# Kernel tuning notes

Hardware: AMD Instinct MI355X
Metric: run time of the kernel (lower is better)

The kernel has to match this reference:

```python
import jax, jax.numpy as jnp
import numpy as np

N_NODES = 100000


def gcn_conv(x, edge_index, W, b):
    # PyG GCNConv: h = D^{-1/2} (A + I) D^{-1/2} (x @ W) + b
    N = x.shape[0]
    h = x @ W  # [N, C_out]
    loops = jnp.arange(N, dtype=edge_index.dtype)
    src = jnp.concatenate([edge_index[0], loops])
    dst = jnp.concatenate([edge_index[1], loops])
    deg = jax.ops.segment_sum(jnp.ones_like(dst, dtype=h.dtype), dst, num_segments=N)
    inv_sqrt = jnp.where(deg > 0, jax.lax.rsqrt(deg), 0.0)
    norm = inv_sqrt[src] * inv_sqrt[dst]              # [E+N]
    msg = h[src] * norm[:, None]                      # gather + scale
    out = jax.ops.segment_sum(msg, dst, num_segments=N)  # scatter-add
    return out + b


def setup_inputs() -> dict:
    key = jax.random.key(0)
    ks = jax.random.split(key, 6)
    x = jax.random.normal(ks[0], (N_NODES, 4), dtype=jnp.float32)
    edge_index = jax.random.randint(ks[1], (2, 3200000), 0, N_NODES, dtype=jnp.int32)
    edge_label_index = jax.random.randint(ks[2], (2, 200000), 0, N_NODES, dtype=jnp.int32)
    W1 = jax.random.normal(ks[3], (4, 128), dtype=jnp.float32) * (1.0 / np.sqrt(4))
    b1 = jnp.zeros((128,), dtype=jnp.float32)
    W2 = jax.random.normal(ks[4], (128, 64), dtype=jnp.float32) * (1.0 / np.sqrt(128))
    b2 = jnp.zeros((64,), dtype=jnp.float32)
    return {"x": x, "edge_index": edge_index, "edge_label_index": edge_label_index,
            "W1": W1, "b1": b1, "W2": W2, "b2": b2}


def reference(x, edge_index, edge_label_index, W1, b1, W2, b2):
    h = jax.nn.relu(gcn_conv(x, edge_index, W1, b1))
    z = gcn_conv(h, edge_index, W2, b2)               # encode -> [N, 64]
    # decode: dot product per labeled edge -> [E_lbl]
    logits = jnp.sum(z[edge_label_index[0]] * z[edge_label_index[1]], axis=-1)
    return logits
```

## Files before the change

### kernel.cpp

```cpp
#include <hip/hip_runtime.h>

#define N_NODES 100000
#define N_EDGES 3200000
#define N_LBL   200000
#define C1 128
#define C2 64

#define BSH   7
#define NPB   128
#define NBKT  ((N_NODES + NPB - 1) / NPB)
#define NCB   500
#define PPT   512
#define CHUNK (N_EDGES / NCB)
#define CAP   4992

#define RS    136

typedef _Float16 half8 __attribute__((ext_vector_type(8)));
typedef float    f32x4 __attribute__((ext_vector_type(4)));

__device__ __forceinline__ float4 f4add(float4 a, float4 b) {
    return make_float4(a.x + b.x, a.y + b.y, a.z + b.z, a.w + b.w);
}
__device__ __forceinline__ unsigned short f2bf(float f) {
    unsigned int u = __float_as_uint(f);
    u += 0x7fff + ((u >> 16) & 1);
    return (unsigned short)(u >> 16);
}
__device__ __forceinline__ float bflo(unsigned int u) {
    return __uint_as_float(u << 16);
}
__device__ __forceinline__ float bfhi(unsigned int u) {
    return __uint_as_float(u & 0xffff0000u);
}
__device__ __forceinline__ void acc16(float* acc, uint4 v) {
    acc[0] += bflo(v.x); acc[1] += bfhi(v.x);
    acc[2] += bflo(v.y); acc[3] += bfhi(v.y);
    acc[4] += bflo(v.z); acc[5] += bfhi(v.z);
    acc[6] += bflo(v.w); acc[7] += bfhi(v.w);
}

__global__ __launch_bounds__(PPT) void pair_place_kernel(const int* __restrict__ ei,
        int* __restrict__ gcursor, unsigned int* __restrict__ pairs) {
    __shared__ int hist[NBKT];
    __shared__ int cur[NBKT];
    __shared__ int lofs[NBKT];
    __shared__ unsigned int sortbuf[CHUNK];
    __shared__ unsigned short bkt16[CHUNK];
    int tid = threadIdx.x;
    for (int i = tid; i < NBKT; i += PPT) hist[i] = 0;
    __syncthreads();
    int base = blockIdx.x * CHUNK;
    unsigned int pk[13]; int bkt[13]; int rnk[13];
    int e0 = base + tid * 12;
    #pragma unroll
    for (int kk = 0; kk < 3; ++kk) {
        int4 sv = *(const int4*)(ei + e0 + kk * 4);
        int4 dv = *(const int4*)(ei + N_EDGES + e0 + kk * 4);
        int b0 = dv.x >> BSH, b1 = dv.y >> BSH;
        int b2 = dv.z >> BSH, b3 = dv.w >> BSH;
        bkt[kk * 4 + 0] = b0;
        pk[kk * 4 + 0] = ((unsigned int)(dv.x & (NPB - 1)) << 17) | (unsigned int)sv.x;
        rnk[kk * 4 + 0] = atomicAdd(&hist[b0], 1);
        bkt[kk * 4 + 1] = b1;
        pk[kk * 4 + 1] = ((unsigned int)(dv.y & (NPB - 1)) << 17) | (unsigned int)sv.y;
        rnk[kk * 4 + 1] = atomicAdd(&hist[b1], 1);
        bkt[kk * 4 + 2] = b2;
        pk[kk * 4 + 2] = ((unsigned int)(dv.z & (NPB - 1)) << 17) | (unsigned int)sv.z;
        rnk[kk * 4 + 2] = atomicAdd(&hist[b2], 1);
        bkt[kk * 4 + 3] = b3;
        pk[kk * 4 + 3] = ((unsigned int)(dv.w & (NPB - 1)) << 17) | (unsigned int)sv.w;
        rnk[kk * 4 + 3] = atomicAdd(&hist[b3], 1);
    }
    if (tid < 256) {
        int e = base + 6144 + tid;
        int s = ei[e], d = ei[N_EDGES + e];
        int b = d >> BSH;
        bkt[12] = b;
        pk[12] = ((unsigned int)(d & (NPB - 1)) << 17) | (unsigned int)s;
        rnk[12] = atomicAdd(&hist[b], 1);
    }
    __syncthreads();
    for (int i = tid; i < NBKT; i += PPT) {
        int h = hist[i];
        cur[i] = h ? (i * CAP + atomicAdd(&gcursor[i], h)) : 0;
    }
    if (tid < 64) {
        int beg = tid * 13;
        int en = min(beg + 13, NBKT);
        int s = 0;
        for (int i = beg; i < en; ++i) s += hist[i];
        int incl = s;
        #pragma unroll
        for (int off = 1; off < 64; off <<= 1) {
            int t = __shfl_up(incl, off);
            if (tid >= off) incl += t;
        }
        int excl = incl - s;
        for (int i = beg; i < en; ++i) {
            lofs[i] = excl;
            excl += hist[i];
        }
    }
    __syncthreads();
    #pragma unroll
    for (int k = 0; k < 12; ++k) {
        int p = lofs[bkt[k]] + rnk[k];
        sortbuf[p] = pk[k];
        bkt16[p] = (unsigned short)bkt[k];
    }
    if (tid < 256) {
        int p = lofs[bkt[12]] + rnk[12];
        sortbuf[p] = pk[12];
        bkt16[p] = (unsigned short)bkt[12];
    }
    __syncthreads();
    for (int j = tid; j < CHUNK; j += PPT) {
        int b = bkt16[j];
        int pos = cur[b] + (j - lofs[b]);
        pos = min(pos, NBKT * CAP - 1);
        pairs[pos] = sortbuf[j];
    }
}

__global__ __launch_bounds__(512) void bucket_finish_kernel(
        const unsigned int* __restrict__ pairs, const int* __restrict__ gcursor,
        const float4* __restrict__ x, int* __restrict__ offs, int* __restrict__ ends,
        float* __restrict__ inv, float4* __restrict__ xs, int* __restrict__ srcs) {
    __shared__ int deg[NPB];
    __shared__ int nstart[NPB];
    __shared__ int wsum2[2];
    __shared__ __align__(16) int ls[CAP];
    int tid = threadIdx.x;
    int b = blockIdx.x;
    int nbase = b << BSH;
    int eb = b * CAP;
    int cnt = min(gcursor[b], CAP);
    if (tid < NPB) deg[tid] = 0;
    __syncthreads();
    unsigned int pk[12]; int rnk[12];
    const uint4* pv = (const uint4*)(pairs + eb);
    #pragma unroll
    for (int kk = 0; kk < 3; ++kk) {
        int j4 = kk * 512 + tid;
        if (kk < 2 || j4 < CAP / 4) {
            uint4 p4 = pv[j4];
            int jb = j4 * 4;
            if (jb < cnt) {
                pk[kk * 4 + 0] = p4.x;
                rnk[kk * 4 + 0] = atomicAdd(&deg[p4.x >> 17], 1);
            }
            if (jb + 1 < cnt) {
                pk[kk * 4 + 1] = p4.y;
                rnk[kk * 4 + 1] = atomicAdd(&deg[p4.y >> 17], 1);
            }
            if (jb + 2 < cnt) {
                pk[kk * 4 + 2] = p4.z;
                rnk[kk * 4 + 2] = atomicAdd(&deg[p4.z >> 17], 1);
            }
            if (jb + 3 < cnt) {
                pk[kk * 4 + 3] = p4.w;
                rnk[kk * 4 + 3] = atomicAdd(&deg[p4.w >> 17], 1);
            }
        }
    }
    __syncthreads();
    int v = 0, incl = 0;
    if (tid < NPB) {
        int lane = tid & 63;
        v = deg[tid];
        incl = v;
        #pragma unroll
        for (int off = 1; off < 64; off <<= 1) {
            int t = __shfl_up(incl, off);
            if (lane >= off) incl += t;
        }
        if (lane == 63) wsum2[tid >> 6] = incl;
    }
    __syncthreads();
    if (tid < NPB) {
        int excl = incl - v + ((tid >= 64) ? wsum2[0] : 0);
        int start = eb + excl;
        nstart[tid] = start;
        int n = nbase + tid;
        if (n < N_NODES) {
            offs[n] = start;
            ends[n] = start + v;
            float iv = rsqrtf((float)(v + 1));
            inv[n] = iv;
            float4 xv = x[n];
            xv.x *= iv; xv.y *= iv; xv.z *= iv; xv.w *= iv;
            xs[n] = xv;
        }
    }
    __syncthreads();
    #pragma unroll
    for (int kk = 0; kk < 3; ++kk) {
        int j4 = kk * 512 + tid;
        int jb = j4 * 4;
        #pragma unroll
        for (int u = 0; u < 4; ++u) {
            if (jb + u < cnt) {
                unsigned int p = pk[kk * 4 + u];
                int lp = nstart[p >> 17] - eb + rnk[kk * 4 + u];
                lp = min(lp, CAP - 1);
                ls[lp] = (int)(p & 0x1FFFFu);
            }
        }
    }
    __syncthreads();
    int cnt4 = (cnt + 3) >> 2;
    for (int i = tid; i < cnt4; i += 512)
        ((int4*)(srcs + eb))[i] = ((const int4*)ls)[i];
}

__global__ __launch_bounds__(256) void agg1_gemm12_kernel(
        const float4* __restrict__ xs, const int* __restrict__ offs,
        const int* __restrict__ ends, const int* __restrict__ srcs,
        const float* __restrict__ inv, const float* __restrict__ W1,
        const float* __restrict__ b1, const float* __restrict__ W2,
        unsigned short* __restrict__ hs2b) {
    __shared__ float w1s[4 * C1];
    __shared__ float bs[C1];
    __shared__ _Float16 w2t[C2 * RS];
    __shared__ _Float16 rows[64 * RS];
    int tid = threadIdx.x;
    int base = blockIdx.x * 64;
    w1s[tid] = W1[tid];
    w1s[tid + 256] = W1[tid + 256];
    if (tid < C1) bs[tid] = b1[tid];
    for (int i = tid; i < C1 * C2; i += 256) {
        int k = i >> 6, n = i & 63;
        w2t[n * RS + k] = (_Float16)W2[i];
    }
    int nd = tid >> 2, g = tid & 3;
    int n = base + nd;
    float4 acc0 = make_float4(0.f, 0.f, 0.f, 0.f);
    {
        if (n < N_NODES) {
            if (g == 0) acc0 = xs[n];
            int e = ends[n];
            for (int j = offs[n] + g; j < e; j += 4)
                acc0 = f4add(acc0, xs[srcs[j]]);
        }
        acc0.x += __shfl_xor(acc0.x, 1); acc0.y += __shfl_xor(acc0.y, 1);
        acc0.z += __shfl_xor(acc0.z, 1); acc0.w += __shfl_xor(acc0.w, 1);
        acc0.x += __shfl_xor(acc0.x, 2); acc0.y += __shfl_xor(acc0.y, 2);
        acc0.z += __shfl_xor(acc0.z, 2); acc0.w += __shfl_xor(acc0.w, 2);
    }
    __syncthreads();
    {
        float s = (n < N_NODES) ? inv[n] : 0.f;
        float4 t = acc0;
        t.x *= s; t.y *= s; t.z *= s; t.w *= s;
        #pragma unroll 8
        for (int cc = 0; cc < 32; ++cc) {
            int c = g + 4 * cc;
            float h = t.x * w1s[c] + t.y * w1s[C1 + c] + t.z * w1s[2 * C1 + c]
                    + t.w * w1s[3 * C1 + c] + bs[c];
            rows[nd * RS + c] = (_Float16)fmaxf(h, 0.f);
        }
    }
    __syncthreads();
    {
        int w = tid >> 6, lane = tid & 63;
        int lm = lane & 15, lg = lane >> 4;
        f32x4 acc[4];
        #pragma unroll
        for (int ct = 0; ct < 4; ++ct) acc[ct] = (f32x4){0.f, 0.f, 0.f, 0.f};
        const _Float16* arow = &rows[(16 * w + lm) * RS + 8 * lg];
        #pragma unroll
        for (int ks = 0; ks < 4; ++ks) {
            half8 a = *(const half8*)(arow + 32 * ks);
            #pragma unroll
            for (int ct = 0; ct < 4; ++ct) {
                half8 b = *(const half8*)(&w2t[(16 * ct + lm) * RS + 8 * lg + 32 * ks]);
                acc[ct] = __builtin_amdgcn_mfma_f32_16x16x32_f16(a, b, acc[ct], 0, 0, 0);
            }
        }
        #pragma unroll
        for (int r = 0; r < 4; ++r) {
            int m = base + 16 * w + 4 * lg + r;
            if (m < N_NODES) {
                float s = inv[m];
                #pragma unroll
                for (int ct = 0; ct < 4; ++ct) {
                    hs2b[(size_t)m * C2 + 16 * ct + lm] = f2bf(acc[ct][r] * s);
                }
            }
        }
    }
}

__global__ void agg2_kernel(const unsigned short* __restrict__ hs2b,
                            const int* __restrict__ offs, const int* __restrict__ ends,
                            const int* __restrict__ srcs, const float* __restrict__ inv,
                            const float4* __restrict__ b2,
                            unsigned short* __restrict__ zb) {
    int gid = blockIdx.x * blockDim.x + threadIdx.x;
    int n = gid >> 6;
    if (n >= N_NODES) return;
    int lane = gid & 63;
    int q = lane & 7;
    int g = lane >> 3;
    float acc[8] = {0.f, 0.f, 0.f, 0.f, 0.f, 0.f, 0.f, 0.f};
    if (g == 0) {
        acc16(acc, *((const uint4*)(hs2b + (size_t)n * C2) + q));
    }
    int e = ends[n];
    int j = offs[n] + g;
    for (; j + 8 < e; j += 16) {
        int s0 = srcs[j];
        int s1 = srcs[j + 8];
        uint4 v0 = *((const uint4*)(hs2b + (size_t)s0 * C2) + q);
        uint4 v1 = *((const uint4*)(hs2b + (size_t)s1 * C2) + q);
        acc16(acc, v0);
        acc16(acc, v1);
    }
    if (j < e) {
        acc16(acc, *((const uint4*)(hs2b + (size_t)srcs[j] * C2) + q));
    }
    #pragma unroll
    for (int k = 0; k < 8; ++k) {
        acc[k] += __shfl_xor(acc[k], 8);
        acc[k] += __shfl_xor(acc[k], 16);
        acc[k] += __shfl_xor(acc[k], 32);
    }
    if (g == 0) {
        float s = inv[n];
        float4 b0 = b2[q * 2], b1v = b2[q * 2 + 1];
        float o0 = acc[0] * s + b0.x,  o1 = acc[1] * s + b0.y;
        float o2 = acc[2] * s + b0.z,  o3 = acc[3] * s + b0.w;
        float o4 = acc[4] * s + b1v.x, o5 = acc[5] * s + b1v.y;
        float o6 = acc[6] * s + b1v.z, o7 = acc[7] * s + b1v.w;
        uint4 w;
        w.x = (unsigned int)f2bf(o0) | ((unsigned int)f2bf(o1) << 16);
        w.y = (unsigned int)f2bf(o2) | ((unsigned int)f2bf(o3) << 16);
        w.z = (unsigned int)f2bf(o4) | ((unsigned int)f2bf(o5) << 16);
        w.w = (unsigned int)f2bf(o6) | ((unsigned int)f2bf(o7) << 16);
        ((uint4*)(zb + (size_t)n * C2))[q] = w;
    }
}

__global__ void decode_kernel(const int* __restrict__ eli,
                              const unsigned short* __restrict__ zb,
                              float* __restrict__ out) {
    int gid = blockIdx.x * blockDim.x + threadIdx.x;
    int e = gid >> 3;
    if (e >= N_LBL) return;
    int q = gid & 7;
    int a = eli[e], b = eli[N_LBL + e];
    uint4 va = ((const uint4*)zb)[(size_t)a * 8 + q];
    uint4 vb = ((const uint4*)zb)[(size_t)b * 8 + q];
    float p = bflo(va.x) * bflo(vb.x) + bfhi(va.x) * bfhi(vb.x)
            + bflo(va.y) * bflo(vb.y) + bfhi(va.y) * bfhi(vb.y)
            + bflo(va.z) * bflo(vb.z) + bfhi(va.z) * bfhi(vb.z)
            + bflo(va.w) * bflo(vb.w) + bfhi(va.w) * bfhi(vb.w);
    p += __shfl_xor(p, 4);
    p += __shfl_xor(p, 2);
    p += __shfl_xor(p, 1);
    if (q == 0) out[e] = p;
}

extern "C" void kernel_launch(void* const* d_in, const int* in_sizes, int n_in,
                              void* d_out, int out_size, void* d_ws, size_t ws_size,
                              hipStream_t stream) {
    const float* x  = (const float*)d_in[0];
    const int*   ei = (const int*)d_in[1];
    const int*  eli = (const int*)d_in[2];
    const float* W1 = (const float*)d_in[3];
    const float* b1 = (const float*)d_in[4];
    const float* W2 = (const float*)d_in[5];
    const float* b2 = (const float*)d_in[6];
    float* out = (float*)d_out;

    char* p = (char*)d_ws;
    int*   gcursor = (int*)p;   p += 1024 * 4;
    int*   offs    = (int*)p;   p += (size_t)N_NODES * 4;
    int*   ends    = (int*)p;   p += (size_t)N_NODES * 4;
    float* inv     = (float*)p; p += (size_t)N_NODES * 4;
    unsigned int* pairs = (unsigned int*)p; p += (size_t)NBKT * CAP * 4;
    int*   srcs    = (int*)p;   p += (size_t)NBKT * CAP * 4;
    float* xs      = (float*)p; p += (size_t)N_NODES * 16;
    unsigned short* hs2b = (unsigned short*)p; p += (size_t)N_NODES * C2 * 2;
    unsigned short* zb   = (unsigned short*)p; p += (size_t)N_NODES * C2 * 2;

    (void)hipMemsetAsync(gcursor, 0, NBKT * 4, stream);
    pair_place_kernel<<<NCB, PPT, 0, stream>>>(ei, gcursor, pairs);
    bucket_finish_kernel<<<NBKT, 512, 0, stream>>>(pairs, gcursor, (const float4*)x,
                                                   offs, ends, inv, (float4*)xs, srcs);
    agg1_gemm12_kernel<<<(N_NODES + 63) / 64, 256, 0, stream>>>(
        (const float4*)xs, offs, ends, srcs, inv, W1, b1, W2, hs2b);
    agg2_kernel<<<((size_t)N_NODES * 64 + 255) / 256, 256, 0, stream>>>(
        hs2b, offs, ends, srcs, inv, (const float4*)b2, zb);
    decode_kernel<<<((size_t)N_LBL * 8 + 255) / 256, 256, 0, stream>>>(eli, zb, out);
}
```

Measured before the change: 212.8 us.

## Replace global-atomic bucket scatter with per-chunk sorted writes and histogram tables

The first pass now writes each chunk's locally bucket-sorted pairs contiguously with vector stores, plus per-chunk histogram and offset tables. This replaces the global atomic cursor and scattered per-element writes. The finish kernel reads each bucket's segments from all 500 chunks, one thread per chunk, walking each short segment serially. That removes the memset and the global atomics, but the reads become many small uncoalesced ones and the finish kernel now makes two passes over its pairs.

```diff
diff --git a/kernel.cpp b/kernel.cpp
--- a/kernel.cpp
+++ b/kernel.cpp
@@ -41,12 +41,11 @@
 }
 
 __global__ __launch_bounds__(PPT) void pair_place_kernel(const int* __restrict__ ei,
-        int* __restrict__ gcursor, unsigned int* __restrict__ pairs) {
+        int* __restrict__ hist_g, int* __restrict__ lofs_g,
+        unsigned int* __restrict__ pairs) {
     __shared__ int hist[NBKT];
-    __shared__ int cur[NBKT];
     __shared__ int lofs[NBKT];
-    __shared__ unsigned int sortbuf[CHUNK];
-    __shared__ unsigned short bkt16[CHUNK];
+    __shared__ __align__(16) unsigned int sortbuf[CHUNK];
     int tid = threadIdx.x;
     for (int i = tid; i < NBKT; i += PPT) hist[i] = 0;
     __syncthreads();
@@ -81,10 +80,6 @@
         rnk[12] = atomicAdd(&hist[b], 1);
     }
     __syncthreads();
-    for (int i = tid; i < NBKT; i += PPT) {
-        int h = hist[i];
-        cur[i] = h ? (i * CAP + atomicAdd(&gcursor[i], h)) : 0;
-    }
     if (tid < 64) {
         int beg = tid * 13;
         int en = min(beg + 13, NBKT);
@@ -104,30 +99,30 @@
     }
     __syncthreads();
     #pragma unroll
-    for (int k = 0; k < 12; ++k) {
-        int p = lofs[bkt[k]] + rnk[k];
-        sortbuf[p] = pk[k];
-        bkt16[p] = (unsigned short)bkt[k];
-    }
-    if (tid < 256) {
-        int p = lofs[bkt[12]] + rnk[12];
-        sortbuf[p] = pk[12];
-        bkt16[p] = (unsigned short)bkt[12];
-    }
-    __syncthreads();
-    for (int j = tid; j < CHUNK; j += PPT) {
-        int b = bkt16[j];
-        int pos = cur[b] + (j - lofs[b]);
-        pos = min(pos, NBKT * CAP - 1);
-        pairs[pos] = sortbuf[j];
+    for (int k = 0; k < 12; ++k)
+        sortbuf[lofs[bkt[k]] + rnk[k]] = pk[k];
+    if (tid < 256)
+        sortbuf[lofs[bkt[12]] + rnk[12]] = pk[12];
+    __syncthreads();
+    uint4* pd = (uint4*)(pairs + base);
+    const uint4* ps = (const uint4*)sortbuf;
+    for (int j = tid; j < CHUNK / 4; j += PPT)
+        pd[j] = ps[j];
+    for (int i = tid; i < NBKT; i += PPT) {
+        hist_g[blockIdx.x * NBKT + i] = hist[i];
+        lofs_g[blockIdx.x * NBKT + i] = lofs[i];
     }
 }
 
 __global__ __launch_bounds__(512) void bucket_finish_kernel(
-        const unsigned int* __restrict__ pairs, const int* __restrict__ gcursor,
-        const float4* __restrict__ x, int* __restrict__ offs, int* __restrict__ ends,
-        float* __restrict__ inv, float4* __restrict__ xs, int* __restrict__ srcs) {
+        const unsigned int* __restrict__ pairs, const int* __restrict__ hist_g,
+        const int* __restrict__ lofs_g, const float4* __restrict__ x,
+        int* __restrict__ offs, int* __restrict__ ends, float* __restrict__ inv,
+        float4* __restrict__ xs, int* __restrict__ srcs) {
+    __shared__ int clen[NCB];
+    __shared__ int cstart[NCB];
     __shared__ int deg[NPB];
+    __shared__ int deg2[NPB];
     __shared__ int nstart[NPB];
     __shared__ int wsum2[2];
     __shared__ __align__(16) int ls[CAP];
@@ -135,33 +130,17 @@
     int b = blockIdx.x;
     int nbase = b << BSH;
     int eb = b * CAP;
-    int cnt = min(gcursor[b], CAP);
-    if (tid < NPB) deg[tid] = 0;
-    __syncthreads();
-    unsigned int pk[12]; int rnk[12];
-    const uint4* pv = (const uint4*)(pairs + eb);
-    #pragma unroll
-    for (int kk = 0; kk < 3; ++kk) {
-        int j4 = kk * 512 + tid;
-        if (kk < 2 || j4 < CAP / 4) {
-            uint4 p4 = pv[j4];
-            int jb = j4 * 4;
-            if (jb < cnt) {
-                pk[kk * 4 + 0] = p4.x;
-                rnk[kk * 4 + 0] = atomicAdd(&deg[p4.x >> 17], 1);
-            }
-            if (jb + 1 < cnt) {
-                pk[kk * 4 + 1] = p4.y;
-                rnk[kk * 4 + 1] = atomicAdd(&deg[p4.y >> 17], 1);
-            }
-            if (jb + 2 < cnt) {
-                pk[kk * 4 + 2] = p4.z;
-                rnk[kk * 4 + 2] = atomicAdd(&deg[p4.z >> 17], 1);
-            }
-            if (jb + 3 < cnt) {
-                pk[kk * 4 + 3] = p4.w;
-                rnk[kk * 4 + 3] = atomicAdd(&deg[p4.w >> 17], 1);
-            }
+    if (tid < NPB) { deg[tid] = 0; deg2[tid] = 0; }
+    if (tid < NCB) {
+        clen[tid] = hist_g[tid * NBKT + b];
+        cstart[tid] = tid * CHUNK + lofs_g[tid * NBKT + b];
+    }
+    __syncthreads();
+    if (tid < NCB) {
+        int cs = cstart[tid], cl = clen[tid];
+        for (int k = 0; k < cl; ++k) {
+            int node = (int)((pairs[cs + k] >> 17) & 127u);
+            atomicAdd(&deg[node], 1);
         }
     }
     __syncthreads();
@@ -194,21 +173,19 @@
         }
     }
     __syncthreads();
-    #pragma unroll
-    for (int kk = 0; kk < 3; ++kk) {
-        int j4 = kk * 512 + tid;
-        int jb = j4 * 4;
-        #pragma unroll
-        for (int u = 0; u < 4; ++u) {
-            if (jb + u < cnt) {
-                unsigned int p = pk[kk * 4 + u];
-                int lp = nstart[p >> 17] - eb + rnk[kk * 4 + u];
-                lp = min(lp, CAP - 1);
-                ls[lp] = (int)(p & 0x1FFFFu);
-            }
-        }
-    }
-    __syncthreads();
+    if (tid < NCB) {
+        int cs = cstart[tid], cl = clen[tid];
+        for (int k = 0; k < cl; ++k) {
+            unsigned int p = pairs[cs + k];
+            int node = (int)((p >> 17) & 127u);
+            int rnk = atomicAdd(&deg2[node], 1);
+            int lp = nstart[node] - eb + rnk;
+            lp = min(lp, CAP - 1);
+            ls[lp] = (int)(p & 0x1FFFFu);
+        }
+    }
+    __syncthreads();
+    int cnt = min(wsum2[0] + wsum2[1], CAP);
     int cnt4 = (cnt + 3) >> 2;
     for (int i = tid; i < cnt4; i += 512)
         ((int4*)(srcs + eb))[i] = ((const int4*)ls)[i];
@@ -375,19 +352,20 @@
     float* out = (float*)d_out;
 
     char* p = (char*)d_ws;
-    int*   gcursor = (int*)p;   p += 1024 * 4;
+    int*   hist_g  = (int*)p;   p += (size_t)NCB * NBKT * 4;
+    int*   lofs_g  = (int*)p;   p += (size_t)NCB * NBKT * 4;
     int*   offs    = (int*)p;   p += (size_t)N_NODES * 4;
     int*   ends    = (int*)p;   p += (size_t)N_NODES * 4;
     float* inv     = (float*)p; p += (size_t)N_NODES * 4;
-    unsigned int* pairs = (unsigned int*)p; p += (size_t)NBKT * CAP * 4;
+    unsigned int* pairs = (unsigned int*)p; p += (size_t)NCB * CHUNK * 4;
     int*   srcs    = (int*)p;   p += (size_t)NBKT * CAP * 4;
     float* xs      = (float*)p; p += (size_t)N_NODES * 16;
     unsigned short* hs2b = (unsigned short*)p; p += (size_t)N_NODES * C2 * 2;
     unsigned short* zb   = (unsigned short*)p; p += (size_t)N_NODES * C2 * 2;
 
-    (void)hipMemsetAsync(gcursor, 0, NBKT * 4, stream);
-    pair_place_kernel<<<NCB, PPT, 0, stream>>>(ei, gcursor, pairs);
-    bucket_finish_kernel<<<NBKT, 512, 0, stream>>>(pairs, gcursor, (const float4*)x,
+    pair_place_kernel<<<NCB, PPT, 0, stream>>>(ei, hist_g, lofs_g, pairs);
+    bucket_finish_kernel<<<NBKT, 512, 0, stream>>>(pairs, hist_g, lofs_g,
+                                                   (const float4*)x,
                                                    offs, ends, inv, (float4*)xs, srcs);
     agg1_gemm12_kernel<<<(N_NODES + 63) / 64, 256, 0, stream>>>(
         (const float4*)xs, offs, ends, srcs, inv, W1, b1, W2, hs2b);
```

Measured after the change: 263.6 us. 1.24x slower.
